# Optimization experiments

Hardware: AMD Instinct MI355X
Metric: run time of the kernel (lower is better)

The kernel has to match this reference:

```python
import jax, jax.numpy as jnp
import numpy as np

V, E, H2, TAG = 32000, 128, 256, 9
H = H2 // 2          # per-direction LSTM hidden
B, T = 128, 512


def setup_inputs() -> dict:
    key = jax.random.key(0)
    ks = jax.random.split(key, 15)
    s = 0.08
    n = lambda k, shp: jax.random.normal(k, shp, dtype=jnp.float32) * s
    return {
        "sentence": jax.random.randint(ks[0], (B, T), 0, V, dtype=jnp.int32),
        "tags": jax.random.randint(ks[1], (B, T), 0, TAG, dtype=jnp.int32),
        "mask": jnp.ones((B, T), dtype=bool),
        "embedding": n(ks[2], (V, E)),
        "w_ih_f": n(ks[3], (4 * H, E)),
        "w_hh_f": n(ks[4], (4 * H, H)),
        "b_f": n(ks[5], (4 * H,)),
        "w_ih_b": n(ks[6], (4 * H, E)),
        "w_hh_b": n(ks[7], (4 * H, H)),
        "b_b": n(ks[8], (4 * H,)),
        "w_out": n(ks[9], (TAG, H2)),
        "b_out": n(ks[10], (TAG,)),
        "start_trans": n(ks[11], (TAG,)),
        "end_trans": n(ks[12], (TAG,)),
        "trans": n(ks[13], (TAG, TAG)),
    }


def _lstm_dir(xp, w_hh):
    """xp: [T,B,4H] precomputed input projections (incl. bias). Returns h seq [T,B,H]."""
    Hn = w_hh.shape[1]
    Bn = xp.shape[1]

    def step(carry, x_t):
        h, c = carry
        g = x_t + h @ w_hh.T                       # [B,4H]
        i, f, gg, o = jnp.split(g, 4, axis=-1)     # torch gate order: i,f,g,o
        c = jax.nn.sigmoid(f) * c + jax.nn.sigmoid(i) * jnp.tanh(gg)
        h = jax.nn.sigmoid(o) * jnp.tanh(c)
        return (h, c), h

    init = (jnp.zeros((Bn, Hn), xp.dtype), jnp.zeros((Bn, Hn), xp.dtype))
    _, hs = jax.lax.scan(step, init, xp)
    return hs


def reference(sentence, tags, mask, embedding, w_ih_f, w_hh_f, b_f,
              w_ih_b, w_hh_b, b_b, w_out, b_out, start_trans, end_trans, trans):
    # ---- BiLSTM emissions ----
    x = embedding[sentence]                 # [B,T,E]
    xt = jnp.swapaxes(x, 0, 1)              # [T,B,E]
    h_f = _lstm_dir(xt @ w_ih_f.T + b_f, w_hh_f)                 # [T,B,H]
    h_b = _lstm_dir((xt @ w_ih_b.T + b_b)[::-1], w_hh_b)[::-1]   # [T,B,H]
    hcat = jnp.concatenate([h_f, h_b], axis=-1)                  # [T,B,2H]
    emissions = hcat @ w_out.T + b_out                           # [T,B,TAG]

    m = mask.T.astype(emissions.dtype)      # [T,B]
    tt = tags.T                             # [T,B]
    bidx = jnp.arange(tt.shape[1])

    # ---- CRF numerator (score of gold path), torchcrf semantics ----
    num0 = start_trans[tt[0]] + emissions[0, bidx, tt[0]]        # [B]

    def num_step(score, inp):
        e_t, t_prev, t_cur, m_t = inp
        return score + (trans[t_prev, t_cur] + e_t[bidx, t_cur]) * m_t, None

    num, _ = jax.lax.scan(num_step, num0, (emissions[1:], tt[:-1], tt[1:], m[1:]))
    seq_ends = mask.sum(axis=1).astype(jnp.int32) - 1            # [B]
    last_tags = tt[seq_ends, bidx]
    num = num + end_trans[last_tags]

    # ---- CRF log-partition (forward algorithm) ----
    alpha0 = start_trans + emissions[0]                          # [B,TAG]

    def fwd_step(alpha, inp):
        e_t, m_t = inp
        nxt = jax.nn.logsumexp(alpha[:, :, None] + trans[None] + e_t[:, None, :], axis=1)
        return jnp.where(m_t[:, None] > 0, nxt, alpha), None

    alpha, _ = jax.lax.scan(fwd_step, alpha0, (emissions[1:], m[1:]))
    logZ = jax.nn.logsumexp(alpha + end_trans, axis=1)           # [B]

    # forward returns -crf(...) with reduction='mean' => mean negative log-likelihood
    return -jnp.mean(num - logZ)
```

## Files before the change

kernel.cpp:

```cpp
#include <hip/hip_runtime.h>
#include <hip/hip_bf16.h>
#include <cstdint>
#include <cstddef>

#define NB   128
#define NT   512
#define NE   128
#define NH   128
#define NG   512
#define NTAG 9

typedef __bf16 bf16;
typedef __bf16 bf16x4 __attribute__((ext_vector_type(4)));
typedef __bf16 bf16x8 __attribute__((ext_vector_type(8)));
typedef _Float16 f16;
typedef _Float16 f16x2 __attribute__((ext_vector_type(2)));
typedef _Float16 f16x8 __attribute__((ext_vector_type(8)));
typedef float  floatx4 __attribute__((ext_vector_type(4)));

__device__ __forceinline__ float bflo_f32(unsigned u) {
  union { unsigned x; float f; } c; c.x = u << 16; return c.f;
}
__device__ __forceinline__ float bfhi_f32(unsigned u) {
  union { unsigned x; float f; } c; c.x = u & 0xFFFF0000u; return c.f;
}
__device__ __forceinline__ f16x2 pkh(float a, float b) {
  return __builtin_bit_cast(f16x2, __builtin_amdgcn_cvt_pkrtz(a, b));
}
__device__ __forceinline__ void block_sync_lds() {
  asm volatile("s_waitcnt lgkmcnt(0)\n\ts_barrier" ::: "memory");
}

__device__ __forceinline__ f16x2 sigm_h(f16x2 x) {
  const f16x2 lo = {(f16)(-2.5f), (f16)(-2.5f)}, hi = {(f16)2.5f, (f16)2.5f};
  x = __builtin_elementwise_min(__builtin_elementwise_max(x, lo), hi);
  f16x2 t = x * x;
  f16x2 p = t * (f16)0.0010154f + (f16)(-0.019144f);
  p = t * p + (f16)0.24964f;
  return x * p + (f16)0.5f;
}
__device__ __forceinline__ f16x2 tanh_h(f16x2 x) {
  const f16x2 lo = {(f16)(-1.5f), (f16)(-1.5f)}, hi = {(f16)1.5f, (f16)1.5f};
  x = __builtin_elementwise_min(__builtin_elementwise_max(x, lo), hi);
  f16x2 t = x * x;
  f16x2 p = t * (f16)0.045172f + (f16)(-0.27334f);
  p = t * p + (f16)0.98976f;
  return x * p;
}

__global__ __launch_bounds__(256, 1) void k_prep(
    const float* __restrict__ emb, const float* __restrict__ w_ih_f,
    const float* __restrict__ w_ih_b, const int* __restrict__ sentence,
    bf16* __restrict__ embb, bf16* __restrict__ wihf, bf16* __restrict__ wihb,
    int* __restrict__ sentT)
{
  const int gid = blockIdx.x * 256 + threadIdx.x;
  const int gsz = gridDim.x * 256;
  for (int i = gid; i < 512000; i += gsz) {
    const float* s = emb + (size_t)i * 8;
    bf16x8 v;
    #pragma unroll
    for (int j = 0; j < 8; ++j) v[j] = (bf16)s[j];
    *(bf16x8*)&embb[(size_t)i * 8] = v;
  }
  for (int i = gid; i < 8192; i += gsz) {
    const float* s = w_ih_f + (size_t)i * 8;
    bf16x8 v;
    #pragma unroll
    for (int j = 0; j < 8; ++j) v[j] = (bf16)s[j];
    *(bf16x8*)&wihf[(size_t)i * 8] = v;
  }
  for (int i = gid; i < 8192; i += gsz) {
    const float* s = w_ih_b + (size_t)i * 8;
    bf16x8 v;
    #pragma unroll
    for (int j = 0; j < 8; ++j) v[j] = (bf16)s[j];
    *(bf16x8*)&wihb[(size_t)i * 8] = v;
  }
  for (int i = gid; i < NT * NB; i += gsz) {
    const int t = i >> 7, b = i & 127;
    sentT[i] = sentence[b * NT + t];
  }
}

__global__ __launch_bounds__(256, 1) void k_embed_proj(
    const int* __restrict__ sentT, const bf16* __restrict__ embb,
    const bf16* __restrict__ wihf, const bf16* __restrict__ wihb,
    const float* __restrict__ b_f, const float* __restrict__ b_b,
    bf16* __restrict__ xp_f, bf16* __restrict__ xp_b)
{
  __shared__ bf16 Cld[128 * 136];
  const int mb = blockIdx.x, nb = blockIdx.y;
  const int colbase = nb * 128;
  const int tid = threadIdx.x;
  const int wv = tid >> 6, lane = tid & 63;
  const int lrow = lane & 15, quad = lane >> 4;
  const int m0 = (wv & 1) * 64, n0 = (wv >> 1) * 64;

  int tokv[4];
  #pragma unroll
  for (int mt = 0; mt < 4; ++mt)
    tokv[mt] = sentT[mb * NB + m0 + mt * 16 + lrow];
  bf16x8 af[4][4];
  #pragma unroll
  for (int kk = 0; kk < 4; ++kk)
    #pragma unroll
    for (int mt = 0; mt < 4; ++mt)
      af[kk][mt] = *(const bf16x8*)&embb[(size_t)tokv[mt] * NE + kk * 32 + quad * 8];

  #pragma unroll
  for (int d = 0; d < 2; ++d) {
    const bf16* W     = (d == 0) ? (wihf + (size_t)nb * 128 * 128)
                                 : (wihb + (size_t)nb * 128 * 128);
    const float* bias = (d == 0) ? (b_f + colbase) : (b_b + colbase);
    bf16* outdir      = (d == 0) ? xp_f : xp_b;

    floatx4 acc[4][4] = {};
    #pragma unroll
    for (int kk = 0; kk < 4; ++kk) {
      bf16x8 bfr[4];
      #pragma unroll
      for (int nt = 0; nt < 4; ++nt)
        bfr[nt] = *(const bf16x8*)&W[(size_t)(n0 + nt * 16 + lrow) * 128 + kk * 32 + quad * 8];
      #pragma unroll
      for (int mt = 0; mt < 4; ++mt)
        #pragma unroll
        for (int nt = 0; nt < 4; ++nt)
          acc[mt][nt] = __builtin_amdgcn_mfma_f32_16x16x32_bf16(af[kk][mt], bfr[nt], acc[mt][nt], 0, 0, 0);
    }
    float bv[4];
    #pragma unroll
    for (int nt = 0; nt < 4; ++nt) bv[nt] = bias[n0 + nt * 16 + lrow];
    if (d == 1) __syncthreads();
    #pragma unroll
    for (int mt = 0; mt < 4; ++mt)
      #pragma unroll
      for (int nt = 0; nt < 4; ++nt) {
        bf16x4 v4;
        #pragma unroll
        for (int rr = 0; rr < 4; ++rr) v4[rr] = (bf16)(acc[mt][nt][rr] + bv[nt]);
        *(bf16x4*)&Cld[(n0 + nt * 16 + lrow) * 136 + m0 + mt * 16 + quad * 4] = v4;
      }
    __syncthreads();
    bf16* outbase = outdir + ((size_t)mb * 8) * (512 * 16) + (size_t)colbase * 16;
    #pragma unroll
    for (int it = 0; it < 8; ++it) {
      const int p = it * 256 + tid;
      const int bb = p >> 8, n = (p >> 1) & 127, half = p & 1;
      *(bf16x8*)(outbase + ((size_t)bb * 512 + n) * 16 + half * 8) =
          *(const bf16x8*)&Cld[n * 136 + bb * 16 + half * 8];
    }
  }
}

#define LSTM_STEP(S, PX, RB, WB)                                               \
  do {                                                                         \
    f16x8 af[4];                                                               \
    _Pragma("unroll")                                                          \
    for (int kk = 0; kk < 4; ++kk)                                             \
      af[kk] = *(const f16x8*)&(RB)[lane * 8 + kk * 512];                      \
    floatx4 acc[4];                                                            \
    _Pragma("unroll")                                                          \
    for (int g = 0; g < 4; ++g) {                                              \
      acc[g][0] = bflo_f32(PX[g][0]); acc[g][1] = bfhi_f32(PX[g][0]);          \
      acc[g][2] = bflo_f32(PX[g][1]); acc[g][3] = bfhi_f32(PX[g][1]);          \
    }                                                                          \
    _Pragma("unroll")                                                          \
    for (int g = 0; g < 4; ++g) {             \
      uint2 u = *(const uint2*)pg[g];                                          \
      PX[g][0] = u.x; PX[g][1] = u.y;                                          \
      pg[g] += dstep_x;                                                        \
    }                                                                          \
    _Pragma("unroll")                                                          \
    for (int kk = 0; kk < 4; ++kk)                                             \
      _Pragma("unroll")                                                        \
      for (int g = 0; g < 4; ++g)                                              \
        acc[g] = __builtin_amdgcn_mfma_f32_16x16x32_f16(af[kk], wf[g][kk],     \
                                                        acc[g], 0, 0, 0);      \
    if (wv == ((S) & 7)) {                    \
      floatx4 eacc = {0.f, 0.f, 0.f, 0.f};                                     \
      _Pragma("unroll")                                                        \
      for (int kk = 0; kk < 4; ++kk)                                           \
        eacc = __builtin_amdgcn_mfma_f32_16x16x32_f16(af[kk], wo[kk],          \
                                                      eacc, 0, 0, 0);          \
      if ((S) > 0 && lrow < NTAG) {                                            \
        ep[eoff + 0] = eacc[0] + bo;  ep[eoff + 9] = eacc[1] + bo;             \
        ep[eoff + 18] = eacc[2] + bo; ep[eoff + 27] = eacc[3] + bo;            \
      }                                                                        \
    }                                                                          \
    {                                                                          \
      f16x2 iv, fv, gv, ov, h2;                                                \
      iv = sigm_h(pkh(acc[0][0], acc[0][1]));                                  \
      fv = sigm_h(pkh(acc[1][0], acc[1][1]));                                  \
      gv = tanh_h(pkh(acc[2][0], acc[2][1]));                                  \
      ov = sigm_h(pkh(acc[3][0], acc[3][1]));                                  \
      c01 = fv * c01 + iv * gv;                                                \
      h2 = ov * tanh_h(c01);                                                   \
      (WB)[wboff + 0 * 8] = h2[0]; (WB)[wboff + 1 * 8] = h2[1];                \
      iv = sigm_h(pkh(acc[0][2], acc[0][3]));                                  \
      fv = sigm_h(pkh(acc[1][2], acc[1][3]));                                  \
      gv = tanh_h(pkh(acc[2][2], acc[2][3]));                                  \
      ov = sigm_h(pkh(acc[3][2], acc[3][3]));                                  \
      c23 = fv * c23 + iv * gv;                                                \
      h2 = ov * tanh_h(c23);                                                   \
      (WB)[wboff + 2 * 8] = h2[0]; (WB)[wboff + 3 * 8] = h2[1];                \
    }                                                                          \
    eoff += destep;                                                            \
    block_sync_lds();                                                          \
  } while (0)

__global__ __launch_bounds__(512, 1) void k_lstm(
    const bf16* __restrict__ xp_f, const bf16* __restrict__ xp_b,
    const float* __restrict__ w_hh_f, const float* __restrict__ w_hh_b,
    const float* __restrict__ w_out, const float* __restrict__ b_out,
    float* __restrict__ eF, float* __restrict__ eB)
{
  __shared__ f16 hfrag[2][2048];
  const int wg = blockIdx.x;
  const int dir = wg >> 3;
  const int bb = wg & 7;
  const int b0 = bb * 16;
  const bf16* __restrict__ xp   = dir ? xp_b   : xp_f;
  const float* __restrict__ Whh = dir ? w_hh_b : w_hh_f;
  float* __restrict__ ep        = dir ? eB     : eF;
  const int tid = threadIdx.x;
  const int wv = tid >> 6, lane = tid & 63;
  const int lrow = lane & 15, quad = lane >> 4;
  const int hc = wv * 16 + lrow;

  f16x8 wf[4][4];
  #pragma unroll
  for (int g = 0; g < 4; ++g)
    #pragma unroll
    for (int kk = 0; kk < 4; ++kk) {
      const float* src = Whh + (size_t)(g * 128 + hc) * 128 + kk * 32 + quad * 8;
      f16x8 v;
      #pragma unroll
      for (int j = 0; j < 8; ++j) v[j] = (f16)src[j];
      wf[g][kk] = v;
    }
  f16x8 wo[4];
  #pragma unroll
  for (int kk = 0; kk < 4; ++kk) {
    f16x8 v;
    #pragma unroll
    for (int j = 0; j < 8; ++j) v[j] = (f16)0.0f;
    if (lrow < NTAG) {
      const float* src = w_out + (size_t)lrow * 256 + dir * 128 + kk * 32 + quad * 8;
      #pragma unroll
      for (int j = 0; j < 8; ++j) v[j] = (f16)src[j];
    }
    wo[kk] = v;
  }
  const float bo = (dir == 0 && lrow < NTAG) ? b_out[lrow] : 0.0f;

  {
    f16x2 z = {(f16)0.f, (f16)0.f};
    *(f16x2*)&hfrag[0][tid * 2] = z;
    *(f16x2*)&hfrag[0][1024 + tid * 2] = z;
  }

  const int t0 = dir ? (NT - 1) : 0;
  const int ddir = dir ? -1 : 1;
  const ptrdiff_t dstep_x = dir ? -(ptrdiff_t)(8 * 512 * 16) : (ptrdiff_t)(8 * 512 * 16);
  const int destep = ddir * (NB * NTAG);
  int eoff = ((t0 - ddir) * NB + b0 + quad * 4) * NTAG + lrow;

  const bf16* pg[4];
  unsigned pxA[4][2], pxB[4][2];
  #pragma unroll
  for (int g = 0; g < 4; ++g)
    pg[g] = xp + (((size_t)t0 * 8 + bb) * 512 + g * 128 + hc) * 16 + quad * 4;
  #pragma unroll
  for (int g = 0; g < 4; ++g) {
    uint2 u = *(const uint2*)pg[g];
    pxA[g][0] = u.x; pxA[g][1] = u.y;
    pg[g] += dstep_x;
  }
  #pragma unroll
  for (int g = 0; g < 4; ++g) {
    uint2 u = *(const uint2*)pg[g];
    pxB[g][0] = u.x; pxB[g][1] = u.y;
    pg[g] += dstep_x;
  }
  const int wboff = ((hc >> 3) * 16 + quad * 4) * 8 + (hc & 7);
  f16x2 c01 = {(f16)0.f, (f16)0.f}, c23 = {(f16)0.f, (f16)0.f};
  block_sync_lds();

  for (int s = 0; s < NT; s += 2) {
    LSTM_STEP(s, pxA, hfrag[0], hfrag[1]);
    LSTM_STEP(s + 1, pxB, hfrag[1], hfrag[0]);
  }
  if (wv == 0) {
    f16x8 afE[4];
    #pragma unroll
    for (int kk = 0; kk < 4; ++kk)
      afE[kk] = *(const f16x8*)&hfrag[0][lane * 8 + kk * 512];
    floatx4 eacc = {0.f, 0.f, 0.f, 0.f};
    #pragma unroll
    for (int kk = 0; kk < 4; ++kk)
      eacc = __builtin_amdgcn_mfma_f32_16x16x32_f16(afE[kk], wo[kk], eacc, 0, 0, 0);
    if (lrow < NTAG) {
      ep[eoff + 0] = eacc[0] + bo;  ep[eoff + 9] = eacc[1] + bo;
      ep[eoff + 18] = eacc[2] + bo; ep[eoff + 27] = eacc[3] + bo;
    }
  }
}

__global__ __launch_bounds__(192, 1) void k_crfA(
    const float* __restrict__ eF, const float* __restrict__ eB,
    const float* __restrict__ trans, float* __restrict__ P)
{
  const int tid = threadIdx.x;
  const int grp = tid >> 4;
  const int j = tid & 15;
  const int c = blockIdx.x;
  const int b = blockIdx.y;
  const int gbase = (tid & 63) & ~15;
  const int i = (grp < 9) ? grp : 8;
  const int jj = (j < NTAG) ? j : 0;

  float tcol[NTAG];
  #pragma unroll
  for (int k = 0; k < NTAG; ++k) tcol[k] = trans[k * NTAG + jj];

  const int t1 = 1 + 8 * c;
  const int nst = (c == 63) ? 6 : 7;
  int eo = (t1 * NB + b) * NTAG + jj;
  float alpha = (j < NTAG) ? (trans[i * NTAG + jj] + eF[eo] + eB[eo]) : -1e30f;
  for (int tt = 0; tt < nst; ++tt) {
    eo += NB * NTAG;
    const float e = eF[eo] + eB[eo];
    float a[NTAG];
    #pragma unroll
    for (int k = 0; k < NTAG; ++k) a[k] = __shfl(alpha, gbase + k, 64) + tcol[k];
    float m = a[0];
    #pragma unroll
    for (int k = 1; k < NTAG; ++k) m = fmaxf(m, a[k]);
    float ssum = 0.0f;
    #pragma unroll
    for (int k = 0; k < NTAG; ++k) ssum += __expf(a[k] - m);
    alpha = m + __logf(ssum) + e;
  }
  if (grp < NTAG && j < NTAG)
    P[(((size_t)b * 64 + c) * NTAG + j) * NTAG + i] = alpha;
}

#define CHUNK_STEP(PC)                                                         \
  do {                                                                         \
    float a[NTAG];                                                             \
    _Pragma("unroll")                                                          \
    for (int k = 0; k < NTAG; ++k) a[k] = __shfl(alpha, gbase + k, 64) + PC[k];\
    float m = a[0];                                                            \
    _Pragma("unroll")                                                          \
    for (int k = 1; k < NTAG; ++k) m = fmaxf(m, a[k]);                         \
    float ssum = 0.0f;                                                         \
    _Pragma("unroll")                                                          \
    for (int k = 0; k < NTAG; ++k) ssum += __expf(a[k] - m);                   \
    alpha = m + __logf(ssum);                                                  \
  } while (0)

__global__ __launch_bounds__(256, 1) void k_crfB(
    const float* __restrict__ eF, const float* __restrict__ eB,
    const int* __restrict__ tags, const float* __restrict__ start_trans,
    const float* __restrict__ end_trans, const float* __restrict__ trans,
    const float* __restrict__ P, float* __restrict__ res)
{
  const int tid = threadIdx.x;
  const int grp = tid >> 4;
  const int j = tid & 15;
  const int b = blockIdx.x * 16 + grp;
  const int gbase = (tid & 63) & ~15;
  const int jj = (j < NTAG) ? j : 0;

  float nsum = 0.0f;
  for (int t = 1 + j; t < NT; t += 16) {
    const int tp = tags[b * NT + t - 1];
    const int tc = tags[b * NT + t];
    const int eo = (t * NB + b) * NTAG + tc;
    nsum += trans[tp * NTAG + tc] + eF[eo] + eB[eo];
  }
  if (j == 0) {
    const int tg0 = tags[b * NT];
    const int tgl = tags[b * NT + NT - 1];
    nsum += start_trans[tg0] + eF[b * NTAG + tg0] + eB[b * NTAG + tg0]
          + end_trans[tgl];
  }
  #pragma unroll
  for (int m = 8; m >= 1; m >>= 1) nsum += __shfl_xor(nsum, m, 16);

  const int e0 = b * NTAG + jj;
  float alpha = (j < NTAG) ? (start_trans[j] + eF[e0] + eB[e0]) : -1e30f;
  const float* Pb = P + ((size_t)b * 64 * 81) + jj * NTAG;
  float pA[NTAG], pB[NTAG];
  #pragma unroll
  for (int k = 0; k < NTAG; ++k) pA[k] = Pb[k];
  #pragma unroll
  for (int k = 0; k < NTAG; ++k) pB[k] = Pb[81 + k];
  for (int c = 0; c < 64; c += 2) {
    CHUNK_STEP(pA);
    if (c + 2 < 64) {
      #pragma unroll
      for (int k = 0; k < NTAG; ++k) pA[k] = Pb[(c + 2) * 81 + k];
    }
    CHUNK_STEP(pB);
    if (c + 3 < 64) {
      #pragma unroll
      for (int k = 0; k < NTAG; ++k) pB[k] = Pb[(c + 3) * 81 + k];
    }
  }
  const float av = (j < NTAG) ? (alpha + end_trans[j]) : -1e30f;
  float vals[NTAG];
  #pragma unroll
  for (int k = 0; k < NTAG; ++k) vals[k] = __shfl(av, gbase + k, 64);
  float m2 = vals[0];
  #pragma unroll
  for (int k = 1; k < NTAG; ++k) m2 = fmaxf(m2, vals[k]);
  float s2 = 0.0f;
  #pragma unroll
  for (int k = 0; k < NTAG; ++k) s2 += __expf(vals[k] - m2);
  const float logZ = m2 + __logf(s2);
  if (j == 0) res[b] = logZ - nsum;
}

__global__ __launch_bounds__(128, 1) void k_mean(const float* __restrict__ res,
                                                 float* __restrict__ out)
{
  const int tid = threadIdx.x;
  float v = res[tid];
  #pragma unroll
  for (int m = 32; m >= 1; m >>= 1) v += __shfl_xor(v, m, 64);
  __shared__ float sv[2];
  if ((tid & 63) == 0) sv[tid >> 6] = v;
  __syncthreads();
  if (tid == 0) out[0] = (sv[0] + sv[1]) * (1.0f / 128.0f);
}

extern "C" void kernel_launch(void* const* d_in, const int* in_sizes, int n_in,
                              void* d_out, int out_size, void* d_ws, size_t ws_size,
                              hipStream_t stream)
{
  (void)in_sizes; (void)n_in; (void)out_size; (void)ws_size;
  const int*   sentence    = (const int*)d_in[0];
  const int*   tags        = (const int*)d_in[1];
  const float* embedding   = (const float*)d_in[3];
  const float* w_ih_f      = (const float*)d_in[4];
  const float* w_hh_f      = (const float*)d_in[5];
  const float* b_f         = (const float*)d_in[6];
  const float* w_ih_b      = (const float*)d_in[7];
  const float* w_hh_b      = (const float*)d_in[8];
  const float* b_b         = (const float*)d_in[9];
  const float* w_out       = (const float*)d_in[10];
  const float* b_out       = (const float*)d_in[11];
  const float* start_trans = (const float*)d_in[12];
  const float* end_trans   = (const float*)d_in[13];
  const float* trans       = (const float*)d_in[14];
  float* out = (float*)d_out;

  char* ws = (char*)d_ws;
  bf16*  xp_f = (bf16*)(ws);
  bf16*  xp_b = (bf16*)(ws + 67108864);
  float* eF   = (float*)(ws + 134217728);
  float* eB   = (float*)(ws + 136577024);
  float* P    = (float*)(ws + 138936320);
  float* res  = (float*)(ws + 141590528);
  bf16*  embb  = (bf16*)(ws + 142606336);
  bf16*  wihf  = (bf16*)(ws + 150994944);
  bf16*  wihb  = (bf16*)(ws + 151126016);
  int*   sentT = (int*) (ws + 151257088);

  k_prep<<<256, 256, 0, stream>>>(embedding, w_ih_f, w_ih_b, sentence,
                                  embb, wihf, wihb, sentT);
  k_embed_proj<<<dim3(512, 4), 256, 0, stream>>>(sentT, embb, wihf, wihb,
                                                 b_f, b_b, xp_f, xp_b);
  k_lstm<<<16, 512, 0, stream>>>(xp_f, xp_b, w_hh_f, w_hh_b, w_out, b_out, eF, eB);
  k_crfA<<<dim3(64, 128), 192, 0, stream>>>(eF, eB, trans, P);
  k_crfB<<<8, 256, 0, stream>>>(eF, eB, tags, start_trans, end_trans, trans, P, res);
  k_mean<<<1, 128, 0, stream>>>(res, out);
}
```

Before: 666.1 us.

## Move emission projection out of the LSTM recurrence into a separate MFMA kernel

The sequential LSTM kernel no longer computes the output projection at each step. Instead it writes the f16 hidden states for both directions to global memory, and a new parallel kernel k_emis computes summed emissions with MFMA. The change takes the extra MFMAs and scattered stores off the latency-bound critical path of the recurrence, and lets the CRF kernels read one emission array instead of two. In exchange it adds about 32 MB of hidden-state writes and reads, one extra kernel launch, and reuses workspace regions for several buffers.

```diff
diff --git a/kernel.cpp b/kernel.cpp
--- a/kernel.cpp
+++ b/kernel.cpp
@@ -153,7 +153,7 @@
   }
 }
 
-#define LSTM_STEP(S, PX, RB, WB)                                               \
+#define LSTM_STEP(PX, RB, WB)                                                  \
   do {                                                                         \
     f16x8 af[4];                                                               \
     _Pragma("unroll")                                                          \
@@ -177,17 +177,6 @@
       for (int g = 0; g < 4; ++g)                                              \
         acc[g] = __builtin_amdgcn_mfma_f32_16x16x32_f16(af[kk], wf[g][kk],     \
                                                         acc[g], 0, 0, 0);      \
-    if (wv == ((S) & 7)) {                    \
-      floatx4 eacc = {0.f, 0.f, 0.f, 0.f};                                     \
-      _Pragma("unroll")                                                        \
-      for (int kk = 0; kk < 4; ++kk)                                           \
-        eacc = __builtin_amdgcn_mfma_f32_16x16x32_f16(af[kk], wo[kk],          \
-                                                      eacc, 0, 0, 0);          \
-      if ((S) > 0 && lrow < NTAG) {                                            \
-        ep[eoff + 0] = eacc[0] + bo;  ep[eoff + 9] = eacc[1] + bo;             \
-        ep[eoff + 18] = eacc[2] + bo; ep[eoff + 27] = eacc[3] + bo;            \
-      }                                                                        \
-    }                                                                          \
     {                                                                          \
       f16x2 iv, fv, gv, ov, h2;                                                \
       iv = sigm_h(pkh(acc[0][0], acc[0][1]));                                  \
@@ -197,6 +186,7 @@
       c01 = fv * c01 + iv * gv;                                                \
       h2 = ov * tanh_h(c01);                                                   \
       (WB)[wboff + 0 * 8] = h2[0]; (WB)[wboff + 1 * 8] = h2[1];                \
+      hop[0 * NH] = h2[0]; hop[1 * NH] = h2[1];                                \
       iv = sigm_h(pkh(acc[0][2], acc[0][3]));                                  \
       fv = sigm_h(pkh(acc[1][2], acc[1][3]));                                  \
       gv = tanh_h(pkh(acc[2][2], acc[2][3]));                                  \
@@ -204,16 +194,16 @@
       c23 = fv * c23 + iv * gv;                                                \
       h2 = ov * tanh_h(c23);                                                   \
       (WB)[wboff + 2 * 8] = h2[0]; (WB)[wboff + 3 * 8] = h2[1];                \
+      hop[2 * NH] = h2[0]; hop[3 * NH] = h2[1];                                \
     }                                                                          \
-    eoff += destep;                                                            \
+    hop += dstep_h;                                                            \
     block_sync_lds();                                                          \
   } while (0)
 
 __global__ __launch_bounds__(512, 1) void k_lstm(
     const bf16* __restrict__ xp_f, const bf16* __restrict__ xp_b,
     const float* __restrict__ w_hh_f, const float* __restrict__ w_hh_b,
-    const float* __restrict__ w_out, const float* __restrict__ b_out,
-    float* __restrict__ eF, float* __restrict__ eB)
+    f16* __restrict__ h_f, f16* __restrict__ h_b)
 {
   __shared__ f16 hfrag[2][2048];
   const int wg = blockIdx.x;
@@ -222,7 +212,7 @@
   const int b0 = bb * 16;
   const bf16* __restrict__ xp   = dir ? xp_b   : xp_f;
   const float* __restrict__ Whh = dir ? w_hh_b : w_hh_f;
-  float* __restrict__ ep        = dir ? eB     : eF;
+  f16* __restrict__ hout        = dir ? h_b    : h_f;
   const int tid = threadIdx.x;
   const int wv = tid >> 6, lane = tid & 63;
   const int lrow = lane & 15, quad = lane >> 4;
@@ -239,21 +229,6 @@
       for (int j = 0; j < 8; ++j) v[j] = (f16)src[j];
       wf[g][kk] = v;
     }
-  f16x8 wo[4];
-  #pragma unroll
-  for (int kk = 0; kk < 4; ++kk) {
-    f16x8 v;
-    #pragma unroll
-    for (int j = 0; j < 8; ++j) v[j] = (f16)0.0f;
-    if (lrow < NTAG) {
-      const float* src = w_out + (size_t)lrow * 256 + dir * 128 + kk * 32 + quad * 8;
-      #pragma unroll
-      for (int j = 0; j < 8; ++j) v[j] = (f16)src[j];
-    }
-    wo[kk] = v;
-  }
-  const float bo = (dir == 0 && lrow < NTAG) ? b_out[lrow] : 0.0f;
-
   {
     f16x2 z = {(f16)0.f, (f16)0.f};
     *(f16x2*)&hfrag[0][tid * 2] = z;
@@ -261,10 +236,8 @@
   }
 
   const int t0 = dir ? (NT - 1) : 0;
-  const int ddir = dir ? -1 : 1;
   const ptrdiff_t dstep_x = dir ? -(ptrdiff_t)(8 * 512 * 16) : (ptrdiff_t)(8 * 512 * 16);
-  const int destep = ddir * (NB * NTAG);
-  int eoff = ((t0 - ddir) * NB + b0 + quad * 4) * NTAG + lrow;
+  const ptrdiff_t dstep_h = dir ? -(ptrdiff_t)(NB * NH) : (ptrdiff_t)(NB * NH);
 
   const bf16* pg[4];
   unsigned pxA[4][2], pxB[4][2];
@@ -283,33 +256,63 @@
     pxB[g][0] = u.x; pxB[g][1] = u.y;
     pg[g] += dstep_x;
   }
+  f16* hop = hout + ((size_t)t0 * NB + b0 + quad * 4) * NH + hc;
   const int wboff = ((hc >> 3) * 16 + quad * 4) * 8 + (hc & 7);
   f16x2 c01 = {(f16)0.f, (f16)0.f}, c23 = {(f16)0.f, (f16)0.f};
   block_sync_lds();
 
   for (int s = 0; s < NT; s += 2) {
-    LSTM_STEP(s, pxA, hfrag[0], hfrag[1]);
-    LSTM_STEP(s + 1, pxB, hfrag[1], hfrag[0]);
-  }
-  if (wv == 0) {
-    f16x8 afE[4];
-    #pragma unroll
-    for (int kk = 0; kk < 4; ++kk)
-      afE[kk] = *(const f16x8*)&hfrag[0][lane * 8 + kk * 512];
-    floatx4 eacc = {0.f, 0.f, 0.f, 0.f};
-    #pragma unroll
-    for (int kk = 0; kk < 4; ++kk)
-      eacc = __builtin_amdgcn_mfma_f32_16x16x32_f16(afE[kk], wo[kk], eacc, 0, 0, 0);
+    LSTM_STEP(pxA, hfrag[0], hfrag[1]);
+    LSTM_STEP(pxB, hfrag[1], hfrag[0]);
+  }
+}
+
+__global__ __launch_bounds__(256, 1) void k_emis(
+    const f16* __restrict__ h_f, const f16* __restrict__ h_b,
+    const float* __restrict__ w_out, const float* __restrict__ b_out,
+    float* __restrict__ emis)
+{
+  const int tid = threadIdx.x;
+  const int wv = tid >> 6, lane = tid & 63;
+  const int lrow = lane & 15, quad = lane >> 4;
+  const int m0 = blockIdx.x * 64 + wv * 16;
+  const size_t mrow = (size_t)(m0 + lrow);
+
+  f16x8 wo[8];
+  #pragma unroll
+  for (int kk = 0; kk < 8; ++kk) {
+    f16x8 v;
+    #pragma unroll
+    for (int j = 0; j < 8; ++j) v[j] = (f16)0.0f;
     if (lrow < NTAG) {
-      ep[eoff + 0] = eacc[0] + bo;  ep[eoff + 9] = eacc[1] + bo;
-      ep[eoff + 18] = eacc[2] + bo; ep[eoff + 27] = eacc[3] + bo;
-    }
+      const float* src = w_out + (size_t)lrow * 256 + kk * 32 + quad * 8;
+      #pragma unroll
+      for (int j = 0; j < 8; ++j) v[j] = (f16)src[j];
+    }
+    wo[kk] = v;
+  }
+  floatx4 acc = {};
+  #pragma unroll
+  for (int kk = 0; kk < 4; ++kk) {
+    const f16x8 a = *(const f16x8*)&h_f[mrow * NH + kk * 32 + quad * 8];
+    acc = __builtin_amdgcn_mfma_f32_16x16x32_f16(a, wo[kk], acc, 0, 0, 0);
+  }
+  #pragma unroll
+  for (int kk = 0; kk < 4; ++kk) {
+    const f16x8 a = *(const f16x8*)&h_b[mrow * NH + kk * 32 + quad * 8];
+    acc = __builtin_amdgcn_mfma_f32_16x16x32_f16(a, wo[kk + 4], acc, 0, 0, 0);
+  }
+  if (lrow < NTAG) {
+    const float bb = b_out[lrow];
+    #pragma unroll
+    for (int rr = 0; rr < 4; ++rr)
+      emis[(size_t)(m0 + quad * 4 + rr) * NTAG + lrow] = acc[rr] + bb;
   }
 }
 
 __global__ __launch_bounds__(192, 1) void k_crfA(
-    const float* __restrict__ eF, const float* __restrict__ eB,
-    const float* __restrict__ trans, float* __restrict__ P)
+    const float* __restrict__ emis, const float* __restrict__ trans,
+    float* __restrict__ P)
 {
   const int tid = threadIdx.x;
   const int grp = tid >> 4;
@@ -327,10 +330,10 @@
   const int t1 = 1 + 8 * c;
   const int nst = (c == 63) ? 6 : 7;
   int eo = (t1 * NB + b) * NTAG + jj;
-  float alpha = (j < NTAG) ? (trans[i * NTAG + jj] + eF[eo] + eB[eo]) : -1e30f;
+  float alpha = (j < NTAG) ? (trans[i * NTAG + jj] + emis[eo]) : -1e30f;
   for (int tt = 0; tt < nst; ++tt) {
     eo += NB * NTAG;
-    const float e = eF[eo] + eB[eo];
+    const float e = emis[eo];
     float a[NTAG];
     #pragma unroll
     for (int k = 0; k < NTAG; ++k) a[k] = __shfl(alpha, gbase + k, 64) + tcol[k];
@@ -361,10 +364,10 @@
   } while (0)
 
 __global__ __launch_bounds__(256, 1) void k_crfB(
-    const float* __restrict__ eF, const float* __restrict__ eB,
-    const int* __restrict__ tags, const float* __restrict__ start_trans,
-    const float* __restrict__ end_trans, const float* __restrict__ trans,
-    const float* __restrict__ P, float* __restrict__ res)
+    const float* __restrict__ emis, const int* __restrict__ tags,
+    const float* __restrict__ start_trans, const float* __restrict__ end_trans,
+    const float* __restrict__ trans, const float* __restrict__ P,
+    float* __restrict__ res)
 {
   const int tid = threadIdx.x;
   const int grp = tid >> 4;
@@ -377,20 +380,17 @@
   for (int t = 1 + j; t < NT; t += 16) {
     const int tp = tags[b * NT + t - 1];
     const int tc = tags[b * NT + t];
-    const int eo = (t * NB + b) * NTAG + tc;
-    nsum += trans[tp * NTAG + tc] + eF[eo] + eB[eo];
+    nsum += trans[tp * NTAG + tc] + emis[(t * NB + b) * NTAG + tc];
   }
   if (j == 0) {
     const int tg0 = tags[b * NT];
     const int tgl = tags[b * NT + NT - 1];
-    nsum += start_trans[tg0] + eF[b * NTAG + tg0] + eB[b * NTAG + tg0]
-          + end_trans[tgl];
+    nsum += start_trans[tg0] + emis[b * NTAG + tg0] + end_trans[tgl];
   }
   #pragma unroll
   for (int m = 8; m >= 1; m >>= 1) nsum += __shfl_xor(nsum, m, 16);
 
-  const int e0 = b * NTAG + jj;
-  float alpha = (j < NTAG) ? (start_trans[j] + eF[e0] + eB[e0]) : -1e30f;
+  float alpha = (j < NTAG) ? (start_trans[j] + emis[b * NTAG + jj]) : -1e30f;
   const float* Pb = P + ((size_t)b * 64 * 81) + jj * NTAG;
   float pA[NTAG], pB[NTAG];
   #pragma unroll
@@ -460,21 +460,23 @@
   char* ws = (char*)d_ws;
   bf16*  xp_f = (bf16*)(ws);
   bf16*  xp_b = (bf16*)(ws + 67108864);
-  float* eF   = (float*)(ws + 134217728);
-  float* eB   = (float*)(ws + 136577024);
-  float* P    = (float*)(ws + 138936320);
-  float* res  = (float*)(ws + 141590528);
-  bf16*  embb  = (bf16*)(ws + 142606336);
-  bf16*  wihf  = (bf16*)(ws + 150994944);
-  bf16*  wihb  = (bf16*)(ws + 151126016);
-  int*   sentT = (int*) (ws + 151257088);
+  f16*   h_f  = (f16*)(ws + 134217728);
+  f16*   h_b  = (f16*)(ws + 150994944);
+  float* emis = (float*)(ws + 167772160);
+  bf16*  embb  = (bf16*)(ws + 134217728);
+  bf16*  wihf  = (bf16*)(ws + 142606336);
+  bf16*  wihb  = (bf16*)(ws + 142737408);
+  int*   sentT = (int*) (ws + 142868480);
+  float* P     = (float*)(ws + 134217728);
+  float* res   = (float*)(ws + 136871936);
 
   k_prep<<<256, 256, 0, stream>>>(embedding, w_ih_f, w_ih_b, sentence,
                                   embb, wihf, wihb, sentT);
   k_embed_proj<<<dim3(512, 4), 256, 0, stream>>>(sentT, embb, wihf, wihb,
                                                  b_f, b_b, xp_f, xp_b);
-  k_lstm<<<16, 512, 0, stream>>>(xp_f, xp_b, w_hh_f, w_hh_b, w_out, b_out, eF, eB);
-  k_crfA<<<dim3(64, 128), 192, 0, stream>>>(eF, eB, trans, P);
-  k_crfB<<<8, 256, 0, stream>>>(eF, eB, tags, start_trans, end_trans, trans, P, res);
+  k_lstm<<<16, 512, 0, stream>>>(xp_f, xp_b, w_hh_f, w_hh_b, h_f, h_b);
+  k_emis<<<1024, 256, 0, stream>>>(h_f, h_b, w_out, b_out, emis);
+  k_crfA<<<dim3(64, 128), 192, 0, stream>>>(emis, trans, P);
+  k_crfB<<<8, 256, 0, stream>>>(emis, tags, start_trans, end_trans, trans, P, res);
   k_mean<<<1, 128, 0, stream>>>(res, out);
 }
```

New measurement: 579.1 us. 13.1% less time.
